# Performance work log

Measured on AMD Instinct MI355X. Metric: run time of the kernel, lower is better.

The kernel has to match this reference:

```python
import jax, jax.numpy as jnp
import numpy as np

B, N, F_IN, F_OUT = 8, 2048, 512, 512


def setup_inputs() -> dict:
    key = jax.random.key(0)
    k1, k2, k3, k4 = jax.random.split(key, 4)
    X = jax.random.normal(k1, (B, N, F_IN), dtype=jnp.float32)
    A = jax.random.uniform(k2, (B, N, N), dtype=jnp.float32)
    # nn.Linear params (kaiming-uniform-ish scale is irrelevant for correctness)
    bound = 1.0 / np.sqrt(F_IN)
    W = jax.random.uniform(k3, (F_IN, F_OUT), dtype=jnp.float32, minval=-bound, maxval=bound)
    b = jax.random.uniform(k4, (F_OUT,), dtype=jnp.float32, minval=-bound, maxval=bound)
    return {"X": X, "A": A, "W": W, "b": b}


def reference(X, A, W, b):
    # A' = A + I  (self-loops)
    A_hat = A + jnp.eye(A.shape[-1], dtype=A.dtype)
    # D^{-1/2}: per-row degree of A'.  torch builds diag_embed + two bmms;
    # mathematically identical to broadcasted row/column scaling.
    d_inv_sqrt = A_hat.sum(axis=-1) ** -0.5                      # [B, N]
    L = A_hat * d_inv_sqrt[:, :, None] * d_inv_sqrt[:, None, :]  # [B, N, N]
    x = X @ W + b                                                # [B, N, F_out]
    return jnp.einsum('bij,bjf->bif', L, x)
```

## Files before the change

kernel.cpp:

```cpp
#include <hip/hip_runtime.h>

#define B_ 8
#define N_ 2048
#define FIN_ 512
#define FOUT_ 512

typedef __attribute__((ext_vector_type(8))) short short8;
typedef __attribute__((ext_vector_type(4))) float floatx4;
typedef __attribute__((ext_vector_type(4))) unsigned short ushortx4;
typedef __attribute__((ext_vector_type(8))) unsigned short ushortx8;

__device__ inline unsigned short f2bf(float f) {
    union { float f; unsigned int u; } x; x.f = f;
    unsigned int r = x.u + 0x7FFFu + ((x.u >> 16) & 1u);
    return (unsigned short)(r >> 16);
}

__device__ inline void glds16(const void* g, void* l) {
    __builtin_amdgcn_global_load_lds(
        (const __attribute__((address_space(1))) void*)g,
        (__attribute__((address_space(3))) void*)l, 16, 0, 0);
}

__global__ __launch_bounds__(256) void degree_cast_kernel(
    const float* __restrict__ A, float* __restrict__ dinv,
    unsigned short* __restrict__ Abf) {
    int row = blockIdx.x;
    size_t base = (size_t)row * N_;
    const float4* A4 = (const float4*)(A + base);
    int t = threadIdx.x;
    float4 v0 = A4[t];
    float4 v1 = A4[t + 256];
    ushortx4 p0, p1;
    p0[0] = f2bf(v0.x); p0[1] = f2bf(v0.y); p0[2] = f2bf(v0.z); p0[3] = f2bf(v0.w);
    p1[0] = f2bf(v1.x); p1[1] = f2bf(v1.y); p1[2] = f2bf(v1.z); p1[3] = f2bf(v1.w);
    *(ushortx4*)(Abf + base + t * 4) = p0;
    *(ushortx4*)(Abf + base + (t + 256) * 4) = p1;
    float s = v0.x + v0.y + v0.z + v0.w + v1.x + v1.y + v1.z + v1.w;
#pragma unroll
    for (int off = 32; off > 0; off >>= 1) s += __shfl_down(s, off, 64);
    __shared__ float red[4];
    if ((t & 63) == 0) red[t >> 6] = s;
    __syncthreads();
    if (t == 0) dinv[row] = rsqrtf(red[0] + red[1] + red[2] + red[3] + 1.0f);
}

__global__ __launch_bounds__(256) void castX_kernel(const float* __restrict__ X,
                                                    unsigned short* __restrict__ Xbf) {
    size_t e0 = ((size_t)blockIdx.x * 256 + threadIdx.x) * 8;
    float4 a0 = *(const float4*)(X + e0);
    float4 a1 = *(const float4*)(X + e0 + 4);
    float av[8] = {a0.x, a0.y, a0.z, a0.w, a1.x, a1.y, a1.z, a1.w};
    ushortx8 p;
#pragma unroll
    for (int r = 0; r < 8; ++r) p[r] = f2bf(av[r]);
    *(ushortx8*)(Xbf + e0) = p;
}

__global__ __launch_bounds__(256) void transposeW_kernel(const float* __restrict__ W,
                                                         unsigned short* __restrict__ Wt) {
    __shared__ float tile[32][33];
    int bx = blockIdx.x * 32;
    int by = blockIdx.y * 32;
    int tx = threadIdx.x, ty = threadIdx.y;
#pragma unroll
    for (int r = 0; r < 32; r += 8)
        tile[ty + r][tx] = W[(size_t)(by + ty + r) * FOUT_ + bx + tx];
    __syncthreads();
#pragma unroll
    for (int r = 0; r < 32; r += 8)
        Wt[(size_t)(bx + ty + r) * FIN_ + by + tx] = f2bf(tile[tx][ty + r]);
}


__global__ __launch_bounds__(256) void gemm1_kernel(
    const unsigned short* __restrict__ Abase,
    const unsigned short* __restrict__ Btbase,
    unsigned short* __restrict__ XwT,
    const float* __restrict__ bias,
    const float* __restrict__ dinv) {
    __shared__ __align__(16) char smem[34816];
    char* As = smem;
    char* Bs = smem + 16384;

    int t = threadIdx.x;
    int lane = t & 63;
    int wave = t >> 6;
    int wr = wave >> 1, wc = wave & 1;
    int q = lane >> 4, m = lane & 15;
    int n0 = blockIdx.x * 128;
    int m0 = blockIdx.y * 128;

    int srow = t >> 3;
    int scol = (((t & 7) ^ (srow & 7)) * 8);
    int x0 = ((q ^ (m & 7)) * 16);
    int x1 = x0 ^ 64;

    floatx4 acc[4][4];
#pragma unroll
    for (int mi = 0; mi < 4; ++mi)
#pragma unroll
        for (int ni = 0; ni < 4; ++ni)
            acc[mi][ni] = (floatx4){0.f, 0.f, 0.f, 0.f};

    const unsigned short* gA = Abase + (size_t)(m0 + srow) * FIN_ + scol;
    const unsigned short* gB = Btbase + (size_t)(n0 + srow) * FIN_ + scol;
    char* lA = As + wave * 1024;
    char* lB = Bs + wave * 1024;

    for (int kt = 0; kt < FIN_ / 64; ++kt) {
#pragma unroll
        for (int u = 0; u < 4; ++u) {
            glds16(gA + (size_t)(u * 32) * FIN_, lA + u * 4096);
            glds16(gB + (size_t)(u * 32) * FIN_, lB + u * 4096);
        }
        gA += 64; gB += 64;
        __syncthreads();

#pragma unroll
        for (int sl = 0; sl < 2; ++sl) {
            int xs = sl ? x1 : x0;
            short8 af[4], bfr[4];
#pragma unroll
            for (int mi = 0; mi < 4; ++mi)
                af[mi] = *(const short8*)(As + (wr * 64 + mi * 16 + m) * 128 + xs);
#pragma unroll
            for (int ni = 0; ni < 4; ++ni)
                bfr[ni] = *(const short8*)(Bs + (wc * 64 + ni * 16 + m) * 128 + xs);
#pragma unroll
            for (int mi = 0; mi < 4; ++mi)
#pragma unroll
                for (int ni = 0; ni < 4; ++ni)
                    acc[mi][ni] = __builtin_amdgcn_mfma_f32_16x16x32_bf16(
                        af[mi], bfr[ni], acc[mi][ni], 0, 0, 0);
        }
        __syncthreads();
    }

    unsigned short* T = (unsigned short*)smem;
#pragma unroll
    for (int mi = 0; mi < 4; ++mi) {
        int row = wr * 64 + mi * 16 + q * 4;
        float4 dv = *(const float4*)(dinv + m0 + row);
        float dr[4] = {dv.x, dv.y, dv.z, dv.w};
#pragma unroll
        for (int ni = 0; ni < 4; ++ni) {
            int col = wc * 64 + ni * 16 + m;
            float bv = bias[n0 + col];
            ushortx4 pk;
#pragma unroll
            for (int r = 0; r < 4; ++r) pk[r] = f2bf((acc[mi][ni][r] + bv) * dr[r]);
            *(ushortx4*)(T + col * 136 + row) = pk;
        }
    }
    __syncthreads();
    int f  = t >> 1;
    int c0 = (t & 1) * 64;
    int bb = m0 >> 11;
    int node0 = (m0 & 2047) + c0;
    unsigned short* dst = XwT + ((size_t)bb * FOUT_ + n0 + f) * N_ + node0;
    const unsigned short* src = T + f * 136 + c0;
#pragma unroll
    for (int u = 0; u < 8; ++u)
        *(ushortx8*)(dst + u * 8) = *(const ushortx8*)(src + u * 8);
}

__global__ __launch_bounds__(256) void gemm2_kernel(
    const unsigned short* __restrict__ Abf,
    const unsigned short* __restrict__ XwT,
    const float* __restrict__ dinv,
    float* __restrict__ out) {
    __shared__ __align__(16) char smem[32768];
    char* As = smem;
    char* Bs = smem + 16384;

    int t = threadIdx.x;
    int lane = t & 63;
    int wave = t >> 6;
    int wr = wave >> 1, wc = wave & 1;
    int q = lane >> 4, m = lane & 15;

    int id = blockIdx.x;
    int b  = id & 7;
    int s  = id >> 3;
    int n0 = (s & 3) * 128;
    int m0 = (s >> 2) * 128;

    const unsigned short* Ab = Abf + (size_t)b * N_ * N_;
    const unsigned short* Bb = XwT + (size_t)b * FOUT_ * N_;

    int srow = t >> 3;
    int scol = (((t & 7) ^ (srow & 7)) * 8);
    int x0 = ((q ^ (m & 7)) * 16);
    int x1 = x0 ^ 64;

    floatx4 acc[4][4];
#pragma unroll
    for (int mi = 0; mi < 4; ++mi)
#pragma unroll
        for (int ni = 0; ni < 4; ++ni)
            acc[mi][ni] = (floatx4){0.f, 0.f, 0.f, 0.f};

    const unsigned short* gA = Ab + (size_t)(m0 + srow) * N_ + scol;
    const unsigned short* gB = Bb + (size_t)(n0 + srow) * N_ + scol;
    char* lA = As + wave * 1024;
    char* lB = Bs + wave * 1024;

    for (int kt = 0; kt < N_ / 64; ++kt) {
#pragma unroll
        for (int u = 0; u < 4; ++u) {
            glds16(gA + (size_t)(u * 32) * N_, lA + u * 4096);
            glds16(gB + (size_t)(u * 32) * N_, lB + u * 4096);
        }
        gA += 64; gB += 64;
        __syncthreads();

#pragma unroll
        for (int sl = 0; sl < 2; ++sl) {
            int xs = sl ? x1 : x0;
            short8 af[4], bfr[4];
#pragma unroll
            for (int mi = 0; mi < 4; ++mi)
                af[mi] = *(const short8*)(As + (wr * 64 + mi * 16 + m) * 128 + xs);
#pragma unroll
            for (int ni = 0; ni < 4; ++ni)
                bfr[ni] = *(const short8*)(Bs + (wc * 64 + ni * 16 + m) * 128 + xs);
#pragma unroll
            for (int mi = 0; mi < 4; ++mi)
#pragma unroll
                for (int ni = 0; ni < 4; ++ni)
                    acc[mi][ni] = __builtin_amdgcn_mfma_f32_16x16x32_bf16(
                        af[mi], bfr[ni], acc[mi][ni], 0, 0, 0);
        }
        __syncthreads();
    }

    float* C = out + (size_t)b * N_ * FOUT_;
#pragma unroll
    for (int mi = 0; mi < 4; ++mi) {
        int rowb = m0 + wr * 64 + mi * 16 + q * 4;
        float4 dv = *(const float4*)(dinv + b * N_ + rowb);
        float dr[4] = {dv.x, dv.y, dv.z, dv.w};
#pragma unroll
        for (int ni = 0; ni < 4; ++ni) {
            int col = n0 + wc * 64 + ni * 16 + m;
            ushortx4 yv = *(const ushortx4*)(Bb + (size_t)col * N_ + rowb);
#pragma unroll
            for (int r = 0; r < 4; ++r) {
                union { unsigned int u; float f; } yc; yc.u = ((unsigned int)yv[r]) << 16;
                C[(size_t)(rowb + r) * FOUT_ + col] = dr[r] * (acc[mi][ni][r] + yc.f);
            }
        }
    }
}

extern "C" void kernel_launch(void* const* d_in, const int* in_sizes, int n_in,
                              void* d_out, int out_size, void* d_ws, size_t ws_size,
                              hipStream_t stream) {
    const float* X    = (const float*)d_in[0];
    const float* A    = (const float*)d_in[1];
    const float* W    = (const float*)d_in[2];
    const float* bias = (const float*)d_in[3];
    float* out = (float*)d_out;
    char* ws = (char*)d_ws;

    float* dinv          = (float*)(ws);
    unsigned short* Xbf  = (unsigned short*)(ws + (1u << 16));
    unsigned short* Wt   = (unsigned short*)(ws + (1u << 16) + 16777216u);
    unsigned short* XwT  = (unsigned short*)(ws + (1u << 16) + 16777216u + 524288u);
    unsigned short* Abf  = (unsigned short*)(ws + (1u << 16) + 16777216u + 524288u + 16777216u);

    degree_cast_kernel<<<B_ * N_, 256, 0, stream>>>(A, dinv, Abf);
    castX_kernel<<<((size_t)B_ * N_ * FIN_) / 2048, 256, 0, stream>>>(X, Xbf);
    transposeW_kernel<<<dim3(FOUT_ / 32, FIN_ / 32), dim3(32, 8), 0, stream>>>(W, Wt);

    gemm1_kernel<<<dim3(FOUT_ / 128, (B_ * N_) / 128), 256, 0, stream>>>(
        Xbf, Wt, XwT, bias, dinv);

    gemm2_kernel<<<512, 256, 0, stream>>>(Abf, XwT, dinv, out);
}
```

Measured before the change: 289.7 us.

## Double-buffer LDS tiles in both GEMM kernels to overlap loads with MFMA

Both GEMM kernels now keep two LDS stages of 32 KB each. While the MFMAs run on the current K-tile, the next tile is already being fetched with global_load_lds into the other buffer, so each iteration needs only one barrier. The goal is to hide global-load latency behind compute. The cost is doubling LDS per block to 64 KB, which can lower the number of blocks resident on each CU.

Measured after the change: 296.4 us. 2.3% more time.

```diff
diff --git a/kernel.cpp b/kernel.cpp
--- a/kernel.cpp
+++ b/kernel.cpp
@@ -79,9 +79,7 @@
     unsigned short* __restrict__ XwT,
     const float* __restrict__ bias,
     const float* __restrict__ dinv) {
-    __shared__ __align__(16) char smem[34816];
-    char* As = smem;
-    char* Bs = smem + 16384;
+    __shared__ __align__(16) char smem[65536];
 
     int t = threadIdx.x;
     int lane = t & 63;
@@ -105,18 +103,33 @@
 
     const unsigned short* gA = Abase + (size_t)(m0 + srow) * FIN_ + scol;
     const unsigned short* gB = Btbase + (size_t)(n0 + srow) * FIN_ + scol;
-    char* lA = As + wave * 1024;
-    char* lB = Bs + wave * 1024;
-
-    for (int kt = 0; kt < FIN_ / 64; ++kt) {
+
+    {
+        char* lA = smem + wave * 1024;
+        char* lB = smem + 16384 + wave * 1024;
 #pragma unroll
         for (int u = 0; u < 4; ++u) {
             glds16(gA + (size_t)(u * 32) * FIN_, lA + u * 4096);
             glds16(gB + (size_t)(u * 32) * FIN_, lB + u * 4096);
         }
         gA += 64; gB += 64;
-        __syncthreads();
-
+    }
+    __syncthreads();
+
+    int cur = 0;
+    for (int kt = 0; kt < FIN_ / 64; ++kt) {
+        if (kt < FIN_ / 64 - 1) {
+            char* lA = smem + (cur ^ 1) * 32768 + wave * 1024;
+            char* lB = smem + (cur ^ 1) * 32768 + 16384 + wave * 1024;
+#pragma unroll
+            for (int u = 0; u < 4; ++u) {
+                glds16(gA + (size_t)(u * 32) * FIN_, lA + u * 4096);
+                glds16(gB + (size_t)(u * 32) * FIN_, lB + u * 4096);
+            }
+            gA += 64; gB += 64;
+        }
+        const char* As = smem + cur * 32768;
+        const char* Bs = As + 16384;
 #pragma unroll
         for (int sl = 0; sl < 2; ++sl) {
             int xs = sl ? x1 : x0;
@@ -135,6 +148,7 @@
                         af[mi], bfr[ni], acc[mi][ni], 0, 0, 0);
         }
         __syncthreads();
+        cur ^= 1;
     }
 
     unsigned short* T = (unsigned short*)smem;
@@ -170,9 +184,7 @@
     const unsigned short* __restrict__ XwT,
     const float* __restrict__ dinv,
     float* __restrict__ out) {
-    __shared__ __align__(16) char smem[32768];
-    char* As = smem;
-    char* Bs = smem + 16384;
+    __shared__ __align__(16) char smem[65536];
 
     int t = threadIdx.x;
     int lane = t & 63;
@@ -203,18 +215,33 @@
 
     const unsigned short* gA = Ab + (size_t)(m0 + srow) * N_ + scol;
     const unsigned short* gB = Bb + (size_t)(n0 + srow) * N_ + scol;
-    char* lA = As + wave * 1024;
-    char* lB = Bs + wave * 1024;
-
-    for (int kt = 0; kt < N_ / 64; ++kt) {
+
+    {
+        char* lA = smem + wave * 1024;
+        char* lB = smem + 16384 + wave * 1024;
 #pragma unroll
         for (int u = 0; u < 4; ++u) {
             glds16(gA + (size_t)(u * 32) * N_, lA + u * 4096);
             glds16(gB + (size_t)(u * 32) * N_, lB + u * 4096);
         }
         gA += 64; gB += 64;
-        __syncthreads();
-
+    }
+    __syncthreads();
+
+    int cur = 0;
+    for (int kt = 0; kt < N_ / 64; ++kt) {
+        if (kt < N_ / 64 - 1) {
+            char* lA = smem + (cur ^ 1) * 32768 + wave * 1024;
+            char* lB = smem + (cur ^ 1) * 32768 + 16384 + wave * 1024;
+#pragma unroll
+            for (int u = 0; u < 4; ++u) {
+                glds16(gA + (size_t)(u * 32) * N_, lA + u * 4096);
+                glds16(gB + (size_t)(u * 32) * N_, lB + u * 4096);
+            }
+            gA += 64; gB += 64;
+        }
+        const char* As = smem + cur * 32768;
+        const char* Bs = As + 16384;
 #pragma unroll
         for (int sl = 0; sl < 2; ++sl) {
             int xs = sl ? x1 : x0;
@@ -233,6 +260,7 @@
                         af[mi], bfr[ni], acc[mi][ni], 0, 0, 0);
         }
         __syncthreads();
+        cur ^= 1;
     }
 
     float* C = out + (size_t)b * N_ * FOUT_;
```

## Double-buffer LDS tiles with async global-to-LDS prefetch in both GEMMs

Applied to the files above, without the earlier changes.

Both GEMM kernels now use two 32KB LDS stages. The tile two k-steps ahead is issued with global_load_lds while the current tile is read into registers and multiplied, and explicit vmcnt/lgkmcnt waits plus barriers replace the old syncthreads pair. The goal is to hide global memory latency behind MFMA work. In exchange, LDS per block doubles to 64KB, which can cut occupancy, and the hand-written waitcnt counts must match the number of loads in flight exactly.

Result: no change. 286.3 us (-1.2%).

```diff
diff --git a/kernel.cpp b/kernel.cpp
--- a/kernel.cpp
+++ b/kernel.cpp
@@ -79,9 +79,7 @@
     unsigned short* __restrict__ XwT,
     const float* __restrict__ bias,
     const float* __restrict__ dinv) {
-    __shared__ __align__(16) char smem[34816];
-    char* As = smem;
-    char* Bs = smem + 16384;
+    __shared__ __align__(16) char smem[65536];
 
     int t = threadIdx.x;
     int lane = t & 63;
@@ -105,37 +103,55 @@
 
     const unsigned short* gA = Abase + (size_t)(m0 + srow) * FIN_ + scol;
     const unsigned short* gB = Btbase + (size_t)(n0 + srow) * FIN_ + scol;
-    char* lA = As + wave * 1024;
-    char* lB = Bs + wave * 1024;
-
-    for (int kt = 0; kt < FIN_ / 64; ++kt) {
-#pragma unroll
-        for (int u = 0; u < 4; ++u) {
-            glds16(gA + (size_t)(u * 32) * FIN_, lA + u * 4096);
-            glds16(gB + (size_t)(u * 32) * FIN_, lB + u * 4096);
-        }
-        gA += 64; gB += 64;
-        __syncthreads();
-
+
+#define STAGE1(bufi) do {                                              \
+        char* lA = smem + (bufi) * 32768 + wave * 1024;                \
+        char* lB = smem + (bufi) * 32768 + 16384 + wave * 1024;        \
+        _Pragma("unroll")                                              \
+        for (int u = 0; u < 4; ++u) {                                  \
+            glds16(gA + (size_t)(u * 32) * FIN_, lA + u * 4096);       \
+            glds16(gB + (size_t)(u * 32) * FIN_, lB + u * 4096);       \
+        }                                                              \
+        gA += 64; gB += 64;                                            \
+    } while (0)
+
+    STAGE1(0);
+    STAGE1(1);
+
+    const int NT = FIN_ / 64;
+    for (int kt = 0; kt < NT; ++kt) {
+        if (kt < NT - 1) asm volatile("s_waitcnt vmcnt(8)" ::: "memory");
+        else             asm volatile("s_waitcnt vmcnt(0)" ::: "memory");
+        __builtin_amdgcn_sched_barrier(0);
+        __builtin_amdgcn_s_barrier();
+        const char* As = smem + (kt & 1) * 32768;
+        const char* Bs = As + 16384;
+        short8 af[2][4], bfr[2][4];
 #pragma unroll
         for (int sl = 0; sl < 2; ++sl) {
             int xs = sl ? x1 : x0;
-            short8 af[4], bfr[4];
 #pragma unroll
             for (int mi = 0; mi < 4; ++mi)
-                af[mi] = *(const short8*)(As + (wr * 64 + mi * 16 + m) * 128 + xs);
+                af[sl][mi] = *(const short8*)(As + (wr * 64 + mi * 16 + m) * 128 + xs);
 #pragma unroll
             for (int ni = 0; ni < 4; ++ni)
-                bfr[ni] = *(const short8*)(Bs + (wc * 64 + ni * 16 + m) * 128 + xs);
+                bfr[sl][ni] = *(const short8*)(Bs + (wc * 64 + ni * 16 + m) * 128 + xs);
+        }
+        asm volatile("s_waitcnt lgkmcnt(0)" ::: "memory");
+        __builtin_amdgcn_sched_barrier(0);
+        __builtin_amdgcn_s_barrier();
+        if (kt + 2 < NT) STAGE1(kt & 1);
+        __builtin_amdgcn_sched_barrier(0);
+#pragma unroll
+        for (int sl = 0; sl < 2; ++sl)
 #pragma unroll
             for (int mi = 0; mi < 4; ++mi)
 #pragma unroll
                 for (int ni = 0; ni < 4; ++ni)
                     acc[mi][ni] = __builtin_amdgcn_mfma_f32_16x16x32_bf16(
-                        af[mi], bfr[ni], acc[mi][ni], 0, 0, 0);
-        }
-        __syncthreads();
+                        af[sl][mi], bfr[sl][ni], acc[mi][ni], 0, 0, 0);
     }
+#undef STAGE1
 
     unsigned short* T = (unsigned short*)smem;
 #pragma unroll
@@ -170,9 +186,7 @@
     const unsigned short* __restrict__ XwT,
     const float* __restrict__ dinv,
     float* __restrict__ out) {
-    __shared__ __align__(16) char smem[32768];
-    char* As = smem;
-    char* Bs = smem + 16384;
+    __shared__ __align__(16) char smem[65536];
 
     int t = threadIdx.x;
     int lane = t & 63;
@@ -203,37 +217,55 @@
 
     const unsigned short* gA = Ab + (size_t)(m0 + srow) * N_ + scol;
     const unsigned short* gB = Bb + (size_t)(n0 + srow) * N_ + scol;
-    char* lA = As + wave * 1024;
-    char* lB = Bs + wave * 1024;
-
-    for (int kt = 0; kt < N_ / 64; ++kt) {
-#pragma unroll
-        for (int u = 0; u < 4; ++u) {
-            glds16(gA + (size_t)(u * 32) * N_, lA + u * 4096);
-            glds16(gB + (size_t)(u * 32) * N_, lB + u * 4096);
-        }
-        gA += 64; gB += 64;
-        __syncthreads();
-
+
+#define STAGE2(bufi) do {                                              \
+        char* lA = smem + (bufi) * 32768 + wave * 1024;                \
+        char* lB = smem + (bufi) * 32768 + 16384 + wave * 1024;        \
+        _Pragma("unroll")                                              \
+        for (int u = 0; u < 4; ++u) {                                  \
+            glds16(gA + (size_t)(u * 32) * N_, lA + u * 4096);         \
+            glds16(gB + (size_t)(u * 32) * N_, lB + u * 4096);         \
+        }                                                              \
+        gA += 64; gB += 64;                                            \
+    } while (0)
+
+    STAGE2(0);
+    STAGE2(1);
+
+    const int NT = N_ / 64;
+    for (int kt = 0; kt < NT; ++kt) {
+        if (kt < NT - 1) asm volatile("s_waitcnt vmcnt(8)" ::: "memory");
+        else             asm volatile("s_waitcnt vmcnt(0)" ::: "memory");
+        __builtin_amdgcn_sched_barrier(0);
+        __builtin_amdgcn_s_barrier();
+        const char* As = smem + (kt & 1) * 32768;
+        const char* Bs = As + 16384;
+        short8 af[2][4], bfr[2][4];
 #pragma unroll
         for (int sl = 0; sl < 2; ++sl) {
             int xs = sl ? x1 : x0;
-            short8 af[4], bfr[4];
 #pragma unroll
             for (int mi = 0; mi < 4; ++mi)
-                af[mi] = *(const short8*)(As + (wr * 64 + mi * 16 + m) * 128 + xs);
+                af[sl][mi] = *(const short8*)(As + (wr * 64 + mi * 16 + m) * 128 + xs);
 #pragma unroll
             for (int ni = 0; ni < 4; ++ni)
-                bfr[ni] = *(const short8*)(Bs + (wc * 64 + ni * 16 + m) * 128 + xs);
+                bfr[sl][ni] = *(const short8*)(Bs + (wc * 64 + ni * 16 + m) * 128 + xs);
+        }
+        asm volatile("s_waitcnt lgkmcnt(0)" ::: "memory");
+        __builtin_amdgcn_sched_barrier(0);
+        __builtin_amdgcn_s_barrier();
+        if (kt + 2 < NT) STAGE2(kt & 1);
+        __builtin_amdgcn_sched_barrier(0);
+#pragma unroll
+        for (int sl = 0; sl < 2; ++sl)
 #pragma unroll
             for (int mi = 0; mi < 4; ++mi)
 #pragma unroll
                 for (int ni = 0; ni < 4; ++ni)
                     acc[mi][ni] = __builtin_amdgcn_mfma_f32_16x16x32_bf16(
-                        af[mi], bfr[ni], acc[mi][ni], 0, 0, 0);
-        }
-        __syncthreads();
+                        af[sl][mi], bfr[sl][ni], acc[mi][ni], 0, 0, 0);
     }
+#undef STAGE2
 
     float* C = out + (size_t)b * N_ * FOUT_;
 #pragma unroll
```
